# Optimization experiments

Measured on AMD Instinct MI355X. Metric: run time of the kernel, lower is better.

Reference implementation:

```python
import jax, jax.numpy as jnp
import numpy as np

N_HEAD, F_IN, F_OUT = 4, 768, 64
BS, N = 4, 2048


def setup_inputs() -> dict:
    key = jax.random.key(0)
    k_h, k_w, k_src, k_dst = jax.random.split(key, 4)
    # xavier_uniform bounds
    lim_w = float(np.sqrt(6.0 / (F_IN + F_OUT)))
    lim_a = float(np.sqrt(6.0 / (F_OUT + 1)))
    return {
        "h": jax.random.normal(k_h, (BS, N, F_IN), dtype=jnp.float32),
        "w": jax.random.uniform(k_w, (N_HEAD, F_IN, F_OUT), jnp.float32, -lim_w, lim_w),
        "a_src": jax.random.uniform(k_src, (N_HEAD, F_OUT, 1), jnp.float32, -lim_a, lim_a),
        "a_dst": jax.random.uniform(k_dst, (N_HEAD, F_OUT, 1), jnp.float32, -lim_a, lim_a),
        "bias": jnp.zeros((F_OUT,), dtype=jnp.float32),
    }


def reference(h, w, a_src, a_dst, bias):
    # h: [b, n, f_in]; w: [h, f_in, f_out]
    h_prime = jnp.einsum("bnf,hfo->bhno", h, w)          # [b, h, n, f_out]
    t = jnp.tanh(h_prime)
    attn_src = jnp.einsum("bhno,ho->bhn", t, a_src[..., 0])  # [b, h, n]
    attn_dst = jnp.einsum("bhno,ho->bhn", t, a_dst[..., 0])  # [b, h, n]
    # broadcast add: attn[b,h,i,j] = src[b,h,i] + dst[b,h,j]
    attn = attn_src[..., :, None] + attn_dst[..., None, :]   # [b, h, n, n]
    attn = jnp.where(attn >= 0, attn, 0.2 * attn)            # leaky_relu(0.2)
    attn = jax.nn.softmax(attn, axis=-1)
    out = jnp.einsum("bhij,bhjo->bhio", attn, h_prime)       # [b, h, n, f_out]
    return out + bias
```

## Files before the change

kernel.cpp:

```cpp
#include <hip/hip_runtime.h>
#include <hip/hip_bf16.h>

#define NHEAD 4
#define FIN   768
#define FOUT  64
#define BSZ   4
#define NSEQ  2048
#define BH    (BSZ*NHEAD)

typedef __attribute__((ext_vector_type(8))) short bf16x8;
typedef __attribute__((ext_vector_type(4))) float f32x4;
typedef __attribute__((ext_vector_type(8))) unsigned short u16x8;
typedef __attribute__((ext_vector_type(4))) unsigned short u16x4;

__device__ __forceinline__ unsigned short f2bf(float f){
  unsigned b = __float_as_uint(f);
  return (unsigned short)((b + 0x7fffu + ((b >> 16) & 1u)) >> 16);
}
__device__ __forceinline__ unsigned fenc(float f){
  unsigned b = __float_as_uint(f);
  return (b & 0x80000000u) ? ~b : (b | 0x80000000u);
}
__device__ __forceinline__ float fdec(unsigned u){
  unsigned b = (u & 0x80000000u) ? (u ^ 0x80000000u) : ~u;
  return __uint_as_float(b);
}

__global__ __launch_bounds__(256) void k_prep_w(
    const float* __restrict__ w, unsigned short* __restrict__ wp)
{
  const int head = blockIdx.x, kt = blockIdx.y;
  #pragma unroll
  for (int p = 0; p < 2; ++p){
    int u = threadIdx.x + p*256;
    int o = u >> 3, c = u & 7;
    u16x8 pk;
    #pragma unroll
    for (int j = 0; j < 8; ++j){
      float v = w[((size_t)head*FIN + kt*64 + c*8 + j)*FOUT + o];
      pk[j] = f2bf(v);
    }
    int slot = c ^ (o & 7);
    *(u16x8*)((char*)wp + ((size_t)((head*12 + kt)*64 + o))*128 + slot*16) = pk;
  }
}

__global__ __launch_bounds__(512, 2) void k_hprime(
    const float* __restrict__ h, const unsigned short* __restrict__ wp,
    const float* __restrict__ a_src, const float* __restrict__ a_dst,
    unsigned short* __restrict__ hpz, float* __restrict__ srcv,
    float* __restrict__ dstv, unsigned* __restrict__ dmaxe)
{
  __shared__ __align__(16) char smem[16384];
  char* Ash = smem;
  char* Bsh = smem + 8192;
  const int tid  = threadIdx.x;
  const int i0a  = blockIdx.x * 64;
  const int jbase = i0a & (NSEQ-1);
  const int head = blockIdx.y;
  const int wave = tid >> 6, lane = tid & 63;
  const int wm = (wave >> 1) & 1, wn = wave & 1, kw = wave >> 2;
  const int quad = lane >> 4, l16 = lane & 15;

  f32x4 acc[2][2] = {};

  const int sr = tid >> 3, sc = tid & 7;
  const float* hsrc = h + (size_t)(i0a + sr)*FIN + sc*8;
  const char* wblock = (const char*)wp + (size_t)head*12*8192;

  for (int kt = 0; kt < 12; ++kt){
    float4 v0 = *(const float4*)(hsrc + kt*64);
    float4 v1 = *(const float4*)(hsrc + kt*64 + 4);
    u16x8 pk;
    pk[0]=f2bf(v0.x); pk[1]=f2bf(v0.y); pk[2]=f2bf(v0.z); pk[3]=f2bf(v0.w);
    pk[4]=f2bf(v1.x); pk[5]=f2bf(v1.y); pk[6]=f2bf(v1.z); pk[7]=f2bf(v1.w);
    *(u16x8*)(Ash + sr*128 + ((sc ^ (sr & 7)) << 4)) = pk;
    *(u16x8*)(Bsh + tid*16) = *(const u16x8*)(wblock + (size_t)kt*8192 + tid*16);
    __syncthreads();

    const int fslot = (((kw << 2) + quad) ^ (l16 & 7)) << 4;
    bf16x8 a0 = *(const bf16x8*)(Ash + (wm*32      + l16)*128 + fslot);
    bf16x8 a1 = *(const bf16x8*)(Ash + (wm*32 + 16 + l16)*128 + fslot);
    bf16x8 b0 = *(const bf16x8*)(Bsh + (wn*32      + l16)*128 + fslot);
    bf16x8 b1 = *(const bf16x8*)(Bsh + (wn*32 + 16 + l16)*128 + fslot);
    acc[0][0] = __builtin_amdgcn_mfma_f32_16x16x32_bf16(a0, b0, acc[0][0], 0,0,0);
    acc[0][1] = __builtin_amdgcn_mfma_f32_16x16x32_bf16(a0, b1, acc[0][1], 0,0,0);
    acc[1][0] = __builtin_amdgcn_mfma_f32_16x16x32_bf16(a1, b0, acc[1][0], 0,0,0);
    acc[1][1] = __builtin_amdgcn_mfma_f32_16x16x32_bf16(a1, b1, acc[1][1], 0,0,0);
    __syncthreads();
  }

  if (kw == 1){
    char* scr = smem + ((size_t)(wave & 3)*64 + lane)*64;
    *(f32x4*)(scr     ) = acc[0][0]; *(f32x4*)(scr + 16) = acc[0][1];
    *(f32x4*)(scr + 32) = acc[1][0]; *(f32x4*)(scr + 48) = acc[1][1];
  }
  __syncthreads();
  if (kw == 0){
    char* scr = smem + ((size_t)wave*64 + lane)*64;
    acc[0][0] += *(const f32x4*)(scr     ); acc[0][1] += *(const f32x4*)(scr + 16);
    acc[1][0] += *(const f32x4*)(scr + 32); acc[1][1] += *(const f32x4*)(scr + 48);
  }
  __syncthreads();

  float* psumS = (float*)(smem + 8192);
  float* psumD = psumS + 128;

  if (kw == 0){
    const float as0 = a_src[head*64 + wn*32 + l16];
    const float as1 = a_src[head*64 + wn*32 + 16 + l16];
    const float ad0 = a_dst[head*64 + wn*32 + l16];
    const float ad1 = a_dst[head*64 + wn*32 + 16 + l16];
    #pragma unroll
    for (int mi = 0; mi < 2; ++mi){
      const int rbase = wm*32 + mi*16 + quad*4;
      #pragma unroll
      for (int reg = 0; reg < 4; ++reg){
        float vA = acc[mi][0][reg], vB = acc[mi][1][reg];
        float t0 = tanhf(vA), t1 = tanhf(vB);
        float ps = t0*as0 + t1*as1;
        float pd = t0*ad0 + t1*ad1;
        ps += __shfl_xor(ps, 1); ps += __shfl_xor(ps, 2);
        ps += __shfl_xor(ps, 4); ps += __shfl_xor(ps, 8);
        pd += __shfl_xor(pd, 1); pd += __shfl_xor(pd, 2);
        pd += __shfl_xor(pd, 4); pd += __shfl_xor(pd, 8);
        if (l16 == 0){
          psumS[(rbase + reg)*2 + wn] = ps;
          psumD[(rbase + reg)*2 + wn] = pd;
        }
      }
      #pragma unroll
      for (int ni = 0; ni < 2; ++ni){
        const int orow = wn*32 + ni*16 + l16;
        u16x4 c4;
        c4[0] = f2bf(acc[mi][ni][0]); c4[1] = f2bf(acc[mi][ni][1]);
        c4[2] = f2bf(acc[mi][ni][2]); c4[3] = f2bf(acc[mi][ni][3]);
        const int slot = ((rbase >> 3) & 7) ^ (orow & 7);
        *(u16x4*)(smem + orow*128 + slot*16 + (rbase & 7)*2) = c4;
      }
    }
  }
  __syncthreads();

  const int bh = (i0a >> 11)*NHEAD + head;
  {
    const int o = tid >> 3, part = tid & 7;
    u16x8 val = *(const u16x8*)(smem + o*128 + part*16);
    *(u16x8*)((char*)hpz + ((size_t)(bh*64 + o)*NSEQ + jbase)*2 + part*16) = val;
  }
  if (tid < 64){
    float sv = psumS[tid*2] + psumS[tid*2 + 1];
    float dv = psumD[tid*2] + psumD[tid*2 + 1];
    srcv[(size_t)bh*NSEQ + jbase + tid] = sv;
    dstv[(size_t)bh*NSEQ + jbase + tid] = dv;
    float dmx = dv;
    dmx = fmaxf(dmx, __shfl_xor(dmx, 1));  dmx = fmaxf(dmx, __shfl_xor(dmx, 2));
    dmx = fmaxf(dmx, __shfl_xor(dmx, 4));  dmx = fmaxf(dmx, __shfl_xor(dmx, 8));
    dmx = fmaxf(dmx, __shfl_xor(dmx, 16)); dmx = fmaxf(dmx, __shfl_xor(dmx, 32));
    if (tid == 0) atomicMax(&dmaxe[bh], fenc(dmx));
  }
}

__global__ __launch_bounds__(512, 2) void k_attn(
    const unsigned short* __restrict__ hpz, const float* __restrict__ srcv,
    const float* __restrict__ dstv, const unsigned* __restrict__ dmaxe,
    const float* __restrict__ bias, float* __restrict__ out)
{
  __shared__ __align__(16) char smem[26880];
  float* dsh  = (float*)smem;
  char*  Psh  = smem + 8192;
  char*  Hsh  = smem + 16384;
  float* lsum = (float*)(smem + 24576);
  float* linv = (float*)(smem + 26624);

  const int tid = threadIdx.x;
  const int i0  = blockIdx.x * 64;
  const int bh  = blockIdx.y;
  const int wave = tid >> 6, lane = tid & 63;
  const int wm = (wave >> 1) & 1, wn = wave & 1, kw = wave >> 2;
  const int quad = lane >> 4, l16 = lane & 15;

  *(float4*)(dsh + tid*4) = *(const float4*)(dstv + (size_t)bh*NSEQ + tid*4);

  const int ip = tid >> 3, cch = tid & 7;
  const float s  = srcv[(size_t)bh*NSEQ + i0 + ip];
  const float dm = fdec(dmaxe[bh]);
  float mrow = s + dm; mrow = fmaxf(mrow, 0.2f*mrow);
  float lpart = 0.f;
  f32x4 acc[2][2] = {};
  const int pslot = (cch ^ (ip & 7)) << 4;
  const char* hsrc = (const char*)hpz + (size_t)(bh*64 + ip)*NSEQ*2 + cch*16;
  __syncthreads();

  for (int jt = 0; jt < NSEQ; jt += 64){
    *(u16x8*)(Hsh + tid*16) = *(const u16x8*)(hsrc + jt*2);
    u16x8 pk;
    #pragma unroll
    for (int j = 0; j < 8; ++j){
      float x = s + dsh[jt + cch*8 + j];
      x = fmaxf(x, 0.2f*x);
      float ev = __expf(x - mrow);
      lpart += ev;
      pk[j] = f2bf(ev);
    }
    *(u16x8*)(Psh + ip*128 + pslot) = pk;
    __syncthreads();

    const int fslot = (((kw << 2) + quad) ^ (l16 & 7)) << 4;
    bf16x8 a0 = *(const bf16x8*)(Psh + (wm*32      + l16)*128 + fslot);
    bf16x8 a1 = *(const bf16x8*)(Psh + (wm*32 + 16 + l16)*128 + fslot);
    bf16x8 b0 = *(const bf16x8*)(Hsh + (wn*32      + l16)*128 + fslot);
    bf16x8 b1 = *(const bf16x8*)(Hsh + (wn*32 + 16 + l16)*128 + fslot);
    acc[0][0] = __builtin_amdgcn_mfma_f32_16x16x32_bf16(a0, b0, acc[0][0], 0,0,0);
    acc[0][1] = __builtin_amdgcn_mfma_f32_16x16x32_bf16(a0, b1, acc[0][1], 0,0,0);
    acc[1][0] = __builtin_amdgcn_mfma_f32_16x16x32_bf16(a1, b0, acc[1][0], 0,0,0);
    acc[1][1] = __builtin_amdgcn_mfma_f32_16x16x32_bf16(a1, b1, acc[1][1], 0,0,0);
    __syncthreads();
  }

  lsum[tid] = lpart;
  if (kw == 1){
    char* scr = smem + 8192 + ((size_t)(wave & 3)*64 + lane)*64;
    *(f32x4*)(scr     ) = acc[0][0]; *(f32x4*)(scr + 16) = acc[0][1];
    *(f32x4*)(scr + 32) = acc[1][0]; *(f32x4*)(scr + 48) = acc[1][1];
  }
  __syncthreads();
  if (kw == 0){
    char* scr = smem + 8192 + ((size_t)wave*64 + lane)*64;
    acc[0][0] += *(const f32x4*)(scr     ); acc[0][1] += *(const f32x4*)(scr + 16);
    acc[1][0] += *(const f32x4*)(scr + 32); acc[1][1] += *(const f32x4*)(scr + 48);
  }
  if (tid < 64){
    float l = 0.f;
    #pragma unroll
    for (int c = 0; c < 8; ++c) l += lsum[tid*8 + c];
    linv[tid] = 1.f / l;
  }
  __syncthreads();

  if (kw == 0){
    const float bv0 = bias[wn*32 + l16];
    const float bv1 = bias[wn*32 + 16 + l16];
    #pragma unroll
    for (int mi = 0; mi < 2; ++mi){
      const int ibase = wm*32 + mi*16 + quad*4;
      #pragma unroll
      for (int reg = 0; reg < 4; ++reg){
        const float ri = linv[ibase + reg];
        float* op = out + ((size_t)bh*NSEQ + i0 + ibase + reg)*64;
        op[wn*32      + l16] = acc[mi][0][reg]*ri + bv0;
        op[wn*32 + 16 + l16] = acc[mi][1][reg]*ri + bv1;
      }
    }
  }
}

extern "C" void kernel_launch(void* const* d_in, const int* in_sizes, int n_in,
                              void* d_out, int out_size, void* d_ws, size_t ws_size,
                              hipStream_t stream)
{
  const float* h     = (const float*)d_in[0];
  const float* w     = (const float*)d_in[1];
  const float* a_src = (const float*)d_in[2];
  const float* a_dst = (const float*)d_in[3];
  const float* bias  = (const float*)d_in[4];
  float* out = (float*)d_out;

  char* ws = (char*)d_ws;
  unsigned short* hpz = (unsigned short*)ws;
  float* srcv = (float*)(ws + (4u<<20));
  float* dstv = (float*)(ws + (4u<<20) + (128u<<10));
  unsigned short* wp = (unsigned short*)(ws + (4u<<20) + (256u<<10));
  unsigned* dmaxe = (unsigned*)(ws + (4u<<20) + (640u<<10));

  hipMemsetAsync(dmaxe, 0, BH*sizeof(unsigned), stream);
  k_prep_w<<<dim3(NHEAD, 12), 256, 0, stream>>>(w, wp);
  k_hprime<<<dim3(NSEQ*BSZ/64, NHEAD), 512, 0, stream>>>(h, wp, a_src, a_dst,
                                                         hpz, srcv, dstv, dmaxe);
  k_attn<<<dim3(NSEQ/64, BH), 512, 0, stream>>>(hpz, srcv, dstv, dmaxe, bias, out);
}
```

Measured before the change: 128.2 us.

## Double-buffer LDS with register prefetch and switch to 32x32x16 MFMA tiles

Both the projection and attention kernels now stage two K-tiles per iteration into double-buffered shared memory. Next-tile global loads and exp computation are issued right after the barrier, so they overlap the MFMA work, and one barrier per iteration is dropped. The 16x16x32 MFMA quartet is replaced by a single 32x32x16 accumulator per wave. The dmaxe memset is folded into the weight-prep kernel and the softmax row sums are reduced with shuffles. The trade-off is 64KB of shared memory per block, which may limit occupancy despite launch bounds asking for 4 blocks per CU.

```diff
diff --git a/kernel.cpp b/kernel.cpp
--- a/kernel.cpp
+++ b/kernel.cpp
@@ -8,10 +8,10 @@
 #define NSEQ  2048
 #define BH    (BSZ*NHEAD)
 
-typedef __attribute__((ext_vector_type(8))) short bf16x8;
-typedef __attribute__((ext_vector_type(4))) float f32x4;
-typedef __attribute__((ext_vector_type(8))) unsigned short u16x8;
-typedef __attribute__((ext_vector_type(4))) unsigned short u16x4;
+typedef __attribute__((ext_vector_type(8)))  short bf16x8;
+typedef __attribute__((ext_vector_type(16))) float f32x16;
+typedef __attribute__((ext_vector_type(8)))  unsigned short u16x8;
+typedef __attribute__((ext_vector_type(4)))  unsigned short u16x4;
 
 __device__ __forceinline__ unsigned short f2bf(float f){
   unsigned b = __float_as_uint(f);
@@ -25,10 +25,18 @@
   unsigned b = (u & 0x80000000u) ? (u ^ 0x80000000u) : ~u;
   return __uint_as_float(b);
 }
+__device__ __forceinline__ float pexp(float s, float d, float m){
+  float x = s + d;
+  x = fmaxf(x, 0.2f*x);
+  return __expf(x - m);
+}
 
 __global__ __launch_bounds__(256) void k_prep_w(
-    const float* __restrict__ w, unsigned short* __restrict__ wp)
-{
+    const float* __restrict__ w, unsigned short* __restrict__ wp,
+    unsigned* __restrict__ dmaxe)
+{
+  if (blockIdx.x == 0 && blockIdx.y == 0 && threadIdx.x < BH)
+    dmaxe[threadIdx.x] = 0;
   const int head = blockIdx.x, kt = blockIdx.y;
   #pragma unroll
   for (int p = 0; p < 2; ++p){
@@ -36,118 +44,109 @@
     int o = u >> 3, c = u & 7;
     u16x8 pk;
     #pragma unroll
-    for (int j = 0; j < 8; ++j){
-      float v = w[((size_t)head*FIN + kt*64 + c*8 + j)*FOUT + o];
-      pk[j] = f2bf(v);
-    }
-    int slot = c ^ (o & 7);
-    *(u16x8*)((char*)wp + ((size_t)((head*12 + kt)*64 + o))*128 + slot*16) = pk;
-  }
-}
-
-__global__ __launch_bounds__(512, 2) void k_hprime(
+    for (int j = 0; j < 8; ++j)
+      pk[j] = f2bf(w[((size_t)head*FIN + kt*64 + c*8 + j)*FOUT + o]);
+    *(u16x8*)((char*)wp + ((size_t)((head*12 + kt)*64 + o))*128 + (c ^ (o & 7))*16) = pk;
+  }
+}
+
+__global__ __launch_bounds__(512, 4) void k_hprime(
     const float* __restrict__ h, const unsigned short* __restrict__ wp,
     const float* __restrict__ a_src, const float* __restrict__ a_dst,
     unsigned short* __restrict__ hpz, float* __restrict__ srcv,
     float* __restrict__ dstv, unsigned* __restrict__ dmaxe)
 {
-  __shared__ __align__(16) char smem[16384];
-  char* Ash = smem;
-  char* Bsh = smem + 8192;
+  __shared__ __align__(16) char smem[65536];
+  float* psumS = (float*)(smem + 16384);
+  float* psumD = (float*)(smem + 16896);
+  char*  Tt    = smem + 32768;
+
   const int tid  = threadIdx.x;
   const int i0a  = blockIdx.x * 64;
   const int jbase = i0a & (NSEQ-1);
   const int head = blockIdx.y;
   const int wave = tid >> 6, lane = tid & 63;
-  const int wm = (wave >> 1) & 1, wn = wave & 1, kw = wave >> 2;
-  const int quad = lane >> 4, l16 = lane & 15;
-
-  f32x4 acc[2][2] = {};
+  const int wm = wave & 1, wn = (wave >> 1) & 1, kw = wave >> 2;
+  const int l32 = lane & 31, h32 = lane >> 5;
+
+  f32x16 acc = {0,0,0,0,0,0,0,0,0,0,0,0,0,0,0,0};
 
   const int sr = tid >> 3, sc = tid & 7;
-  const float* hsrc = h + (size_t)(i0a + sr)*FIN + sc*8;
-  const char* wblock = (const char*)wp + (size_t)head*12*8192;
-
-  for (int kt = 0; kt < 12; ++kt){
-    float4 v0 = *(const float4*)(hsrc + kt*64);
-    float4 v1 = *(const float4*)(hsrc + kt*64 + 4);
-    u16x8 pk;
-    pk[0]=f2bf(v0.x); pk[1]=f2bf(v0.y); pk[2]=f2bf(v0.z); pk[3]=f2bf(v0.w);
-    pk[4]=f2bf(v1.x); pk[5]=f2bf(v1.y); pk[6]=f2bf(v1.z); pk[7]=f2bf(v1.w);
-    *(u16x8*)(Ash + sr*128 + ((sc ^ (sr & 7)) << 4)) = pk;
-    *(u16x8*)(Bsh + tid*16) = *(const u16x8*)(wblock + (size_t)kt*8192 + tid*16);
+  const float* hA = h + (size_t)(i0a + sr)*FIN + sc*8;
+  const char*  wB = (const char*)wp + ((size_t)(head*12*64 + sr))*128 + sc*16;
+  const int aslot = (sc ^ (sr & 7)) << 4;
+
+  float4 ra0 = *(const float4*)(hA);
+  float4 ra1 = *(const float4*)(hA + 4);
+  float4 ra2 = *(const float4*)(hA + 64);
+  float4 ra3 = *(const float4*)(hA + 68);
+  u16x8  rb0 = *(const u16x8*)(wB);
+  u16x8  rb1 = *(const u16x8*)(wB + 8192);
+
+  for (int it = 0; it < 6; ++it){
+    char* Ab = smem + (it & 1)*16384;
+    char* Bb = smem + 32768 + (it & 1)*16384;
+    u16x8 pk0, pk1;
+    pk0[0]=f2bf(ra0.x); pk0[1]=f2bf(ra0.y); pk0[2]=f2bf(ra0.z); pk0[3]=f2bf(ra0.w);
+    pk0[4]=f2bf(ra1.x); pk0[5]=f2bf(ra1.y); pk0[6]=f2bf(ra1.z); pk0[7]=f2bf(ra1.w);
+    pk1[0]=f2bf(ra2.x); pk1[1]=f2bf(ra2.y); pk1[2]=f2bf(ra2.z); pk1[3]=f2bf(ra2.w);
+    pk1[4]=f2bf(ra3.x); pk1[5]=f2bf(ra3.y); pk1[6]=f2bf(ra3.z); pk1[7]=f2bf(ra3.w);
+    *(u16x8*)(Ab + sr*256 + aslot)        = pk0;
+    *(u16x8*)(Ab + sr*256 + 128 + aslot)  = pk1;
+    *(u16x8*)(Bb + sr*256 + sc*16)        = rb0;
+    *(u16x8*)(Bb + sr*256 + 128 + sc*16)  = rb1;
     __syncthreads();
-
-    const int fslot = (((kw << 2) + quad) ^ (l16 & 7)) << 4;
-    bf16x8 a0 = *(const bf16x8*)(Ash + (wm*32      + l16)*128 + fslot);
-    bf16x8 a1 = *(const bf16x8*)(Ash + (wm*32 + 16 + l16)*128 + fslot);
-    bf16x8 b0 = *(const bf16x8*)(Bsh + (wn*32      + l16)*128 + fslot);
-    bf16x8 b1 = *(const bf16x8*)(Bsh + (wn*32 + 16 + l16)*128 + fslot);
-    acc[0][0] = __builtin_amdgcn_mfma_f32_16x16x32_bf16(a0, b0, acc[0][0], 0,0,0);
-    acc[0][1] = __builtin_amdgcn_mfma_f32_16x16x32_bf16(a0, b1, acc[0][1], 0,0,0);
-    acc[1][0] = __builtin_amdgcn_mfma_f32_16x16x32_bf16(a1, b0, acc[1][0], 0,0,0);
-    acc[1][1] = __builtin_amdgcn_mfma_f32_16x16x32_bf16(a1, b1, acc[1][1], 0,0,0);
-    __syncthreads();
-  }
-
-  if (kw == 1){
-    char* scr = smem + ((size_t)(wave & 3)*64 + lane)*64;
-    *(f32x4*)(scr     ) = acc[0][0]; *(f32x4*)(scr + 16) = acc[0][1];
-    *(f32x4*)(scr + 32) = acc[1][0]; *(f32x4*)(scr + 48) = acc[1][1];
-  }
+    if (it < 5){
+      const float* an = hA + (it+1)*128;
+      ra0 = *(const float4*)(an);      ra1 = *(const float4*)(an + 4);
+      ra2 = *(const float4*)(an + 64); ra3 = *(const float4*)(an + 68);
+      const char* bn = wB + (size_t)(2*(it+1))*8192;
+      rb0 = *(const u16x8*)(bn);       rb1 = *(const u16x8*)(bn + 8192);
+    }
+    #pragma unroll
+    for (int s = 0; s < 4; ++s){
+      const int slot = (((s*2 + h32) ^ (l32 & 7)) << 4);
+      bf16x8 av = *(const bf16x8*)(Ab + (wm*32 + l32)*256 + kw*128 + slot);
+      bf16x8 bv = *(const bf16x8*)(Bb + (wn*32 + l32)*256 + kw*128 + slot);
+      acc = __builtin_amdgcn_mfma_f32_32x32x16_bf16(av, bv, acc, 0, 0, 0);
+    }
+  }
+
+  if (kw == 1) *(f32x16*)(smem + (size_t)((wave & 3)*64 + lane)*64) = acc;
   __syncthreads();
   if (kw == 0){
-    char* scr = smem + ((size_t)wave*64 + lane)*64;
-    acc[0][0] += *(const f32x4*)(scr     ); acc[0][1] += *(const f32x4*)(scr + 16);
-    acc[1][0] += *(const f32x4*)(scr + 32); acc[1][1] += *(const f32x4*)(scr + 48);
-  }
-  __syncthreads();
-
-  float* psumS = (float*)(smem + 8192);
-  float* psumD = psumS + 128;
-
-  if (kw == 0){
-    const float as0 = a_src[head*64 + wn*32 + l16];
-    const float as1 = a_src[head*64 + wn*32 + 16 + l16];
-    const float ad0 = a_dst[head*64 + wn*32 + l16];
-    const float ad1 = a_dst[head*64 + wn*32 + 16 + l16];
-    #pragma unroll
-    for (int mi = 0; mi < 2; ++mi){
-      const int rbase = wm*32 + mi*16 + quad*4;
+    acc += *(const f32x16*)(smem + (size_t)((wave & 3)*64 + lane)*64);
+    const float as = a_src[head*64 + wn*32 + l32];
+    const float ad = a_dst[head*64 + wn*32 + l32];
+    #pragma unroll
+    for (int rb = 0; rb < 4; ++rb){
+      const int jb = wm*32 + rb*8 + h32*4;
+      u16x4 c4;
       #pragma unroll
-      for (int reg = 0; reg < 4; ++reg){
-        float vA = acc[mi][0][reg], vB = acc[mi][1][reg];
-        float t0 = tanhf(vA), t1 = tanhf(vB);
-        float ps = t0*as0 + t1*as1;
-        float pd = t0*ad0 + t1*ad1;
-        ps += __shfl_xor(ps, 1); ps += __shfl_xor(ps, 2);
-        ps += __shfl_xor(ps, 4); ps += __shfl_xor(ps, 8);
-        pd += __shfl_xor(pd, 1); pd += __shfl_xor(pd, 2);
-        pd += __shfl_xor(pd, 4); pd += __shfl_xor(pd, 8);
-        if (l16 == 0){
-          psumS[(rbase + reg)*2 + wn] = ps;
-          psumD[(rbase + reg)*2 + wn] = pd;
+      for (int q = 0; q < 4; ++q){
+        const float v = acc[rb*4 + q];
+        c4[q] = f2bf(v);
+        const float t = tanhf(v);
+        float ps = t*as, pd = t*ad;
+        ps += __shfl_xor(ps, 1);  ps += __shfl_xor(ps, 2);  ps += __shfl_xor(ps, 4);
+        ps += __shfl_xor(ps, 8);  ps += __shfl_xor(ps, 16);
+        pd += __shfl_xor(pd, 1);  pd += __shfl_xor(pd, 2);  pd += __shfl_xor(pd, 4);
+        pd += __shfl_xor(pd, 8);  pd += __shfl_xor(pd, 16);
+        if (l32 == 0){
+          psumS[(jb + q)*2 + wn] = ps;
+          psumD[(jb + q)*2 + wn] = pd;
         }
       }
-      #pragma unroll
-      for (int ni = 0; ni < 2; ++ni){
-        const int orow = wn*32 + ni*16 + l16;
-        u16x4 c4;
-        c4[0] = f2bf(acc[mi][ni][0]); c4[1] = f2bf(acc[mi][ni][1]);
-        c4[2] = f2bf(acc[mi][ni][2]); c4[3] = f2bf(acc[mi][ni][3]);
-        const int slot = ((rbase >> 3) & 7) ^ (orow & 7);
-        *(u16x4*)(smem + orow*128 + slot*16 + (rbase & 7)*2) = c4;
-      }
+      const int orow = wn*32 + l32;
+      const int slot = ((jb >> 3) & 7) ^ (orow & 7);
+      *(u16x4*)(Tt + orow*128 + slot*16 + (jb & 7)*2) = c4;
     }
   }
   __syncthreads();
 
   const int bh = (i0a >> 11)*NHEAD + head;
-  {
-    const int o = tid >> 3, part = tid & 7;
-    u16x8 val = *(const u16x8*)(smem + o*128 + part*16);
-    *(u16x8*)((char*)hpz + ((size_t)(bh*64 + o)*NSEQ + jbase)*2 + part*16) = val;
-  }
+  *(u16x8*)((char*)hpz + ((size_t)(bh*64 + sr)*NSEQ + jbase)*2 + sc*16)
+      = *(const u16x8*)(Tt + sr*128 + sc*16);
   if (tid < 64){
     float sv = psumS[tid*2] + psumS[tid*2 + 1];
     float dv = psumD[tid*2] + psumD[tid*2 + 1];
@@ -161,95 +160,109 @@
   }
 }
 
-__global__ __launch_bounds__(512, 2) void k_attn(
+__global__ __launch_bounds__(512, 4) void k_attn(
     const unsigned short* __restrict__ hpz, const float* __restrict__ srcv,
     const float* __restrict__ dstv, const unsigned* __restrict__ dmaxe,
     const float* __restrict__ bias, float* __restrict__ out)
 {
-  __shared__ __align__(16) char smem[26880];
-  float* dsh  = (float*)smem;
-  char*  Psh  = smem + 8192;
-  char*  Hsh  = smem + 16384;
-  float* lsum = (float*)(smem + 24576);
-  float* linv = (float*)(smem + 26624);
+  __shared__ __align__(16) char smem[65536];
+  float* lrow = (float*)(smem + 32768);
+  float* linv = (float*)(smem + 33024);
 
   const int tid = threadIdx.x;
   const int i0  = blockIdx.x * 64;
   const int bh  = blockIdx.y;
   const int wave = tid >> 6, lane = tid & 63;
-  const int wm = (wave >> 1) & 1, wn = wave & 1, kw = wave >> 2;
-  const int quad = lane >> 4, l16 = lane & 15;
-
-  *(float4*)(dsh + tid*4) = *(const float4*)(dstv + (size_t)bh*NSEQ + tid*4);
-
+  const int wm = wave & 1, wn = (wave >> 1) & 1, kw = wave >> 2;
+  const int l32 = lane & 31, h32 = lane >> 5;
   const int ip = tid >> 3, cch = tid & 7;
+
   const float s  = srcv[(size_t)bh*NSEQ + i0 + ip];
   const float dm = fdec(dmaxe[bh]);
   float mrow = s + dm; mrow = fmaxf(mrow, 0.2f*mrow);
   float lpart = 0.f;
-  f32x4 acc[2][2] = {};
+
+  const float* dsrc = dstv + (size_t)bh*NSEQ + cch*8;
+  const char*  hsrc = (const char*)hpz + ((size_t)(bh*64 + ip)*NSEQ)*2 + cch*16;
   const int pslot = (cch ^ (ip & 7)) << 4;
-  const char* hsrc = (const char*)hpz + (size_t)(bh*64 + ip)*NSEQ*2 + cch*16;
-  __syncthreads();
-
-  for (int jt = 0; jt < NSEQ; jt += 64){
-    *(u16x8*)(Hsh + tid*16) = *(const u16x8*)(hsrc + jt*2);
-    u16x8 pk;
-    #pragma unroll
-    for (int j = 0; j < 8; ++j){
-      float x = s + dsh[jt + cch*8 + j];
-      x = fmaxf(x, 0.2f*x);
-      float ev = __expf(x - mrow);
-      lpart += ev;
-      pk[j] = f2bf(ev);
-    }
-    *(u16x8*)(Psh + ip*128 + pslot) = pk;
+
+  f32x16 acc = {0,0,0,0,0,0,0,0,0,0,0,0,0,0,0,0};
+
+  u16x8 hA = *(const u16x8*)(hsrc);
+  u16x8 hB = *(const u16x8*)(hsrc + 128);
+  u16x8 pA, pB;
+  {
+    float4 d0 = *(const float4*)(dsrc);
+    float4 d1 = *(const float4*)(dsrc + 4);
+    float4 d2 = *(const float4*)(dsrc + 64);
+    float4 d3 = *(const float4*)(dsrc + 68);
+    float e;
+    e=pexp(s,d0.x,mrow); lpart+=e; pA[0]=f2bf(e);  e=pexp(s,d0.y,mrow); lpart+=e; pA[1]=f2bf(e);
+    e=pexp(s,d0.z,mrow); lpart+=e; pA[2]=f2bf(e);  e=pexp(s,d0.w,mrow); lpart+=e; pA[3]=f2bf(e);
+    e=pexp(s,d1.x,mrow); lpart+=e; pA[4]=f2bf(e);  e=pexp(s,d1.y,mrow); lpart+=e; pA[5]=f2bf(e);
+    e=pexp(s,d1.z,mrow); lpart+=e; pA[6]=f2bf(e);  e=pexp(s,d1.w,mrow); lpart+=e; pA[7]=f2bf(e);
+    e=pexp(s,d2.x,mrow); lpart+=e; pB[0]=f2bf(e);  e=pexp(s,d2.y,mrow); lpart+=e; pB[1]=f2bf(e);
+    e=pexp(s,d2.z,mrow); lpart+=e; pB[2]=f2bf(e);  e=pexp(s,d2.w,mrow); lpart+=e; pB[3]=f2bf(e);
+    e=pexp(s,d3.x,mrow); lpart+=e; pB[4]=f2bf(e);  e=pexp(s,d3.y,mrow); lpart+=e; pB[5]=f2bf(e);
+    e=pexp(s,d3.z,mrow); lpart+=e; pB[6]=f2bf(e);  e=pexp(s,d3.w,mrow); lpart+=e; pB[7]=f2bf(e);
+  }
+
+  for (int it = 0; it < 16; ++it){
+    char* Pb = smem + (it & 1)*16384;
+    char* Hb = smem + 32768 + (it & 1)*16384;
+    *(u16x8*)(Pb + ip*256 + pslot)       = pA;
+    *(u16x8*)(Pb + ip*256 + 128 + pslot) = pB;
+    *(u16x8*)(Hb + ip*256 + cch*16)       = hA;
+    *(u16x8*)(Hb + ip*256 + 128 + cch*16) = hB;
     __syncthreads();
-
-    const int fslot = (((kw << 2) + quad) ^ (l16 & 7)) << 4;
-    bf16x8 a0 = *(const bf16x8*)(Psh + (wm*32      + l16)*128 + fslot);
-    bf16x8 a1 = *(const bf16x8*)(Psh + (wm*32 + 16 + l16)*128 + fslot);
-    bf16x8 b0 = *(const bf16x8*)(Hsh + (wn*32      + l16)*128 + fslot);
-    bf16x8 b1 = *(const bf16x8*)(Hsh + (wn*32 + 16 + l16)*128 + fslot);
-    acc[0][0] = __builtin_amdgcn_mfma_f32_16x16x32_bf16(a0, b0, acc[0][0], 0,0,0);
-    acc[0][1] = __builtin_amdgcn_mfma_f32_16x16x32_bf16(a0, b1, acc[0][1], 0,0,0);
-    acc[1][0] = __builtin_amdgcn_mfma_f32_16x16x32_bf16(a1, b0, acc[1][0], 0,0,0);
-    acc[1][1] = __builtin_amdgcn_mfma_f32_16x16x32_bf16(a1, b1, acc[1][1], 0,0,0);
-    __syncthreads();
-  }
-
-  lsum[tid] = lpart;
-  if (kw == 1){
-    char* scr = smem + 8192 + ((size_t)(wave & 3)*64 + lane)*64;
-    *(f32x4*)(scr     ) = acc[0][0]; *(f32x4*)(scr + 16) = acc[0][1];
-    *(f32x4*)(scr + 32) = acc[1][0]; *(f32x4*)(scr + 48) = acc[1][1];
-  }
-  __syncthreads();
+    if (it < 15){
+      const int jn = (it + 1)*128;
+      hA = *(const u16x8*)(hsrc + jn*2);
+      hB = *(const u16x8*)(hsrc + jn*2 + 128);
+      const float* dn = dsrc + jn;
+      float4 d0 = *(const float4*)(dn);
+      float4 d1 = *(const float4*)(dn + 4);
+      float4 d2 = *(const float4*)(dn + 64);
+      float4 d3 = *(const float4*)(dn + 68);
+      float e;
+      e=pexp(s,d0.x,mrow); lpart+=e; pA[0]=f2bf(e);  e=pexp(s,d0.y,mrow); lpart+=e; pA[1]=f2bf(e);
+      e=pexp(s,d0.z,mrow); lpart+=e; pA[2]=f2bf(e);  e=pexp(s,d0.w,mrow); lpart+=e; pA[3]=f2bf(e);
+      e=pexp(s,d1.x,mrow); lpart+=e; pA[4]=f2bf(e);  e=pexp(s,d1.y,mrow); lpart+=e; pA[5]=f2bf(e);
+      e=pexp(s,d1.z,mrow); lpart+=e; pA[6]=f2bf(e);  e=pexp(s,d1.w,mrow); lpart+=e; pA[7]=f2bf(e);
+      e=pexp(s,d2.x,mrow); lpart+=e; pB[0]=f2bf(e);  e=pexp(s,d2.y,mrow); lpart+=e; pB[1]=f2bf(e);
+      e=pexp(s,d2.z,mrow); lpart+=e; pB[2]=f2bf(e);  e=pexp(s,d2.w,mrow); lpart+=e; pB[3]=f2bf(e);
+      e=pexp(s,d3.x,mrow); lpart+=e; pB[4]=f2bf(e);  e=pexp(s,d3.y,mrow); lpart+=e; pB[5]=f2bf(e);
+      e=pexp(s,d3.z,mrow); lpart+=e; pB[6]=f2bf(e);  e=pexp(s,d3.w,mrow); lpart+=e; pB[7]=f2bf(e);
+    }
+    #pragma unroll
+    for (int st = 0; st < 4; ++st){
+      const int slot = (((st*2 + h32) ^ (l32 & 7)) << 4);
+      bf16x8 av = *(const bf16x8*)(Pb + (wm*32 + l32)*256 + kw*128 + slot);
+      bf16x8 bv = *(const bf16x8*)(Hb + (wn*32 + l32)*256 + kw*128 + slot);
+      acc = __builtin_amdgcn_mfma_f32_32x32x16_bf16(av, bv, acc, 0, 0, 0);
+    }
+  }
+
+  lpart += __shfl_xor(lpart, 1);
+  lpart += __shfl_xor(lpart, 2);
+  lpart += __shfl_xor(lpart, 4);
+  if (cch == 0) lrow[ip] = lpart;
+  if (kw == 1) *(f32x16*)(smem + (size_t)((wave & 3)*64 + lane)*64) = acc;
+  __syncthreads();
+  if (tid < 64) linv[tid] = 1.f / lrow[tid];
+  if (kw == 0)
+    acc += *(const f32x16*)(smem + (size_t)((wave & 3)*64 + lane)*64);
+  __syncthreads();
+
   if (kw == 0){
-    char* scr = smem + 8192 + ((size_t)wave*64 + lane)*64;
-    acc[0][0] += *(const f32x4*)(scr     ); acc[0][1] += *(const f32x4*)(scr + 16);
-    acc[1][0] += *(const f32x4*)(scr + 32); acc[1][1] += *(const f32x4*)(scr + 48);
-  }
-  if (tid < 64){
-    float l = 0.f;
-    #pragma unroll
-    for (int c = 0; c < 8; ++c) l += lsum[tid*8 + c];
-    linv[tid] = 1.f / l;
-  }
-  __syncthreads();
-
-  if (kw == 0){
-    const float bv0 = bias[wn*32 + l16];
-    const float bv1 = bias[wn*32 + 16 + l16];
-    #pragma unroll
-    for (int mi = 0; mi < 2; ++mi){
-      const int ibase = wm*32 + mi*16 + quad*4;
+    const float bv = bias[wn*32 + l32];
+    float* obase = out + ((size_t)bh*NSEQ + i0)*64 + wn*32 + l32;
+    #pragma unroll
+    for (int rb = 0; rb < 4; ++rb){
       #pragma unroll
-      for (int reg = 0; reg < 4; ++reg){
-        const float ri = linv[ibase + reg];
-        float* op = out + ((size_t)bh*NSEQ + i0 + ibase + reg)*64;
-        op[wn*32      + l16] = acc[mi][0][reg]*ri + bv0;
-        op[wn*32 + 16 + l16] = acc[mi][1][reg]*ri + bv1;
+      for (int q = 0; q < 4; ++q){
+        const int irow = wm*32 + rb*8 + h32*4 + q;
+        obase[(size_t)irow*64] = acc[rb*4 + q]*linv[irow] + bv;
       }
     }
   }
@@ -273,8 +286,7 @@
   unsigned short* wp = (unsigned short*)(ws + (4u<<20) + (256u<<10));
   unsigned* dmaxe = (unsigned*)(ws + (4u<<20) + (640u<<10));
 
-  hipMemsetAsync(dmaxe, 0, BH*sizeof(unsigned), stream);
-  k_prep_w<<<dim3(NHEAD, 12), 256, 0, stream>>>(w, wp);
+  k_prep_w<<<dim3(NHEAD, 12), 256, 0, stream>>>(w, wp, dmaxe);
   k_hprime<<<dim3(NSEQ*BSZ/64, NHEAD), 512, 0, stream>>>(h, wp, a_src, a_dst,
                                                          hpz, srcv, dstv, dmaxe);
   k_attn<<<dim3(NSEQ/64, BH), 512, 0, stream>>>(hpz, srcv, dstv, dmaxe, bias, out);
```

After: 125.6 us. 2.1% less time.
